# Optimization experiments

Measured on AMD Instinct MI355X. Metric: run time of the kernel, lower is better.

## Reference

```python
import jax, jax.numpy as jnp
import numpy as np

jax.config.update("jax_enable_x64", True)  # original torch code runs in float64; minors underflow fp32

D = 96   # Nsites
N = 48   # Nparticles


def setup_inputs() -> dict:
    key = jax.random.key(0)
    # Orthonormal single-particle orbitals (columns), as the module assumes (P^T P = I)
    A = jax.random.normal(key, (D, D), dtype=jnp.float64)
    Q, _ = jnp.linalg.qr(A)
    P = Q[:, :N]  # [D, N]
    # A valid ordered particle configuration: strictly increasing, occ_positions[k] <= D-N+k
    occ_positions = jnp.arange(N, dtype=jnp.int32) * (D // N)  # stride-2 filling
    return {"P": P, "occ_positions": occ_positions}


def _cond_probs(P, occ_positions):
    """Conditional probabilities probs[k, x] of placing the k-th (ordered) particle at
    site x given particles 0..k-1 at occ_positions[0..k-1].

    Math identical to SlaterDetSampler_ordered.get_cond_prob (naive_update=True):
      G = I - P P^T
      probs[k,x] = -det(M_x[0:x+1,0:x+1]) / det(M[0:xmin,0:xmin])
    where M = G - diag(occupancy of particles < k) and M_x additionally sets n_x = 1.
    Since Ksites is always the contiguous range 0..x, all determinants are LEADING
    principal minors; and because only the (x,x) diagonal entry changes by -1 (last index
    of the block), det(M_x block) = d_{x+1} - d_x with d_j the leading j-minor of M.
    """
    Dd, Nn = P.shape
    dt = P.dtype
    eye = jnp.eye(Dd, dtype=dt)
    G = eye - P @ P.T                                             # [D, D]

    onehots = jax.nn.one_hot(occ_positions, Dd, dtype=dt)         # [N, D]
    n_before = jnp.cumsum(onehots, axis=0) - onehots              # occupancy of particles < k
    A = G[None] - n_before[:, :, None] * eye                      # [N, D, D]: G - diag(n_<k)

    # All leading principal minors via batched det of masked matrices:
    # M_j = A on the [0:j,0:j] block, identity elsewhere  =>  det(M_j) = leading j-minor
    ii = jnp.arange(Dd)
    jj = jnp.arange(1, Dd + 1)
    blk = (ii[None, :, None] < jj[:, None, None]) & (ii[None, None, :] < jj[:, None, None])  # [D,D,D]
    Ms = jnp.where(blk[None], A[:, None], eye)                    # [N, D, D, D]
    d = jnp.linalg.det(Ms.reshape(Nn * Dd, Dd, Dd)).reshape(Nn, Dd)
    d_full = jnp.concatenate([jnp.ones((Nn, 1), dt), d], axis=1)  # d_full[k, j] = j-th leading minor

    k = jnp.arange(Nn)
    xmin = jnp.where(k == 0, 0, occ_positions[jnp.maximum(k - 1, 0)] + 1)  # [N]
    xmax = Dd - Nn + k + 1                                                  # [N]
    denom = jnp.take_along_axis(d_full, xmin[:, None], axis=1)              # [N, 1]
    num = d_full[:, 1:] - d_full[:, :-1]                                    # det(GG_num) per candidate x

    x = jnp.arange(Dd)
    support = (x[None, :] >= xmin[:, None]) & (x[None, :] < xmax[:, None])
    probs = jnp.where(support, -num / denom, jnp.zeros((), dt))
    # torch.where(abs(probs) > 1e-15, probs, 0.)
    probs = jnp.where(jnp.abs(probs) > 1e-15, probs, jnp.zeros((), dt))
    return probs


def reference(P, occ_positions):
    probs = _cond_probs(P, occ_positions)                          # [N, D]
    # prob of the full ordered sample = prod_k probs[k, occ_positions[k]]  (as in sample())
    p_k = jnp.take_along_axis(probs, occ_positions[:, None], axis=1)[:, 0]
    prob_sample = jnp.prod(p_k)
    return probs, prob_sample
```

## Files before the change

kernel.cpp:

```cpp
#include <hip/hip_runtime.h>
#include <math.h>

#define Dd 96
#define Nn 48
#define LD 97
#define PTS 98
#define WS_G_BYTES (Dd * Dd * 8)

__device__ __forceinline__ double frcp(double x) {
    double r = __builtin_amdgcn_rcp(x);
    r = fma(fma(-x, r, 1.0), r, r);
    r = fma(fma(-x, r, 1.0), r, r);
    return r;
}

__device__ __forceinline__ double rdlane(double v, int srcLane) {
    union { double d; int i[2]; } u; u.d = v;
    int lo = __builtin_amdgcn_readlane(u.i[0], srcLane);
    int hi = __builtin_amdgcn_readlane(u.i[1], srcLane);
    union { int i[2]; double d; } w; w.i[0] = lo; w.i[1] = hi;
    return w.d;
}

__global__ __launch_bounds__(256) void build_g(const float* __restrict__ P,
                                               double* __restrict__ Mg) {
    __shared__ float Ps[Dd * 48];
    const int t0 = threadIdx.x;
    for (int e = t0; e < Dd * 48; e += 256) Ps[e] = P[e];
    __syncthreads();
    const int e = blockIdx.x * 256 + t0;
    const int r = e / Dd, c = e - Dd * (e / Dd);
    const float* pr = Ps + r * 48;
    const float* pc = Ps + c * 48;
    double acc = 0.0;
#pragma unroll
    for (int t = 0; t < 48; ++t)
        acc -= (double)pr[t] * (double)pc[t];
    Mg[e] = acc;
}

__global__ __launch_bounds__(1024, 1) void slater_elim(const double* __restrict__ Mg,
                                                       const int* __restrict__ occ,
                                                       float* __restrict__ out,
                                                       unsigned* __restrict__ cnt) {
    __shared__ double Sbuf[4][6][Dd];
    __shared__ double ev16[16][6];
    __shared__ int    evmask16[16], sdead16[16];
    __shared__ double evm[6];
    __shared__ int    evmmask;
    __shared__ double gs_runprod;
    __shared__ int    gs_dead;
    __shared__ int    step_pub;
    __shared__ int    done4[4];
    __shared__ unsigned char flag[Dd];

    const int tid  = threadIdx.x;
    const int k    = blockIdx.x;
    const int n    = Dd - Nn + k + 1;
    const int lane = tid & 63;
    const int wave = tid >> 6;
    const int xmin = (k == 0) ? 0 : occ[k - 1] + 1;
    const int s_end = (n - 1) / 6;
    const int jend  = 6 * s_end;

    if (tid == 0) { step_pub = -1; gs_runprod = 1.0; gs_dead = 0; evmmask = 0; }
    if (tid < 4)  done4[tid] = 0;
    if (tid < 16) { evmask16[tid] = 0; sdead16[tid] = 0; }
    if (tid < Dd) flag[tid] = 0;
    __syncthreads();
    if (tid < k) flag[occ[tid]] = 1;
    __syncthreads();

    double myprob = 0.0;
    double rr[6][2];

#pragma unroll
    for (int u = 0; u < 6; ++u) {
        if (lane < 48) {
            const int row = 6 * wave + u;
            double2 g = *(const double2*)(Mg + row * Dd + 2 * lane);
            double d0 = (row == 2 * lane     && !flag[row]) ? 1.0 : 0.0;
            double d1 = (row == 2 * lane + 1 && !flag[row]) ? 1.0 : 0.0;
            rr[u][0] = g.x + d0;
            rr[u][1] = g.y + d1;
        } else { rr[u][0] = 0.0; rr[u][1] = 0.0; }
    }

    auto prefactor = [&](int p, int slot) {
        const int jb = 6 * p, jbH = 3 * p;
        double grun = gs_runprod; int gdead = gs_dead;
        int msk = 0;
#pragma unroll
        for (int cc = 0; cc < 6; ++cc) {
            const int src = jbH + (cc >> 1);
            double piv = rdlane(rr[cc][cc & 1], src);
            if (!gdead) {
                double ap = fabs(piv);
                int jj = jb + cc;
                if (jj >= xmin) {
                    if (lane == 0) ev16[p][cc] = grun * (1.0 - piv);
                    msk |= (1 << cc);
                    double nr = grun * piv;
                    if (!(ap > 1e-7) || !(ap < 8.0) || !(fabs(nr) > 1e-8)) gdead = 1;
                    else grun = nr;
                } else {
                    if (!(ap > 1e-12) || !(ap < 8.0)) gdead = 1;
                }
            }
            double rp = frcp(piv);
            rr[cc][0] *= rp; rr[cc][1] *= rp;
#pragma unroll
            for (int i = 0; i < 6; ++i) {
                if (i == cc) continue;
                double f = rdlane(rr[i][cc & 1], src);
                rr[i][0] -= f * rr[cc][0];
                rr[i][1] -= f * rr[cc][1];
            }
        }
        if (lane == 0) {
            evmask16[p] = msk; sdead16[p] = gdead;
            gs_runprod = grun; gs_dead = gdead;
        }
        if (lane < 48) {
            const bool live = (2 * lane >= jb + 6);
#pragma unroll
            for (int r = 0; r < 6; ++r) {
                double2 sv;
                sv.x = live ? rr[r][0] : 0.0;
                sv.y = live ? rr[r][1] : 0.0;
                *(double2*)&Sbuf[slot][r][2 * lane] = sv;
            }
        }
        __threadfence_block();
        if (lane == 0)
            __hip_atomic_store(&step_pub, p, __ATOMIC_RELEASE, __HIP_MEMORY_SCOPE_WORKGROUP);
    };

    if (wave == 0) prefactor(0, 0);

    bool broke = false;
    const int smax = (wave < s_end) ? wave : s_end;
    for (int s = 0; s < smax; ++s) {
        while (__hip_atomic_load(&step_pub, __ATOMIC_ACQUIRE,
                                 __HIP_MEMORY_SCOPE_WORKGROUP) < s)
            __builtin_amdgcn_s_sleep(1);
        if (sdead16[s]) { broke = true; break; }
        const int slot = s & 3;
        double S0[6], S1[6];
        if (lane < 48) {
#pragma unroll
            for (int r = 0; r < 6; ++r) {
                double2 sv = *(const double2*)&Sbuf[slot][r][2 * lane];
                S0[r] = sv.x; S1[r] = sv.y;
            }
        }
        asm volatile("s_waitcnt lgkmcnt(0)" ::: "memory");
        if (lane == 0)
            __hip_atomic_fetch_add(&done4[slot], 1, __ATOMIC_RELAXED,
                                   __HIP_MEMORY_SCOPE_WORKGROUP);
        if (lane < 48) {
            const int al = 3 * s;
#pragma unroll
            for (int u = 0; u < 6; ++u) {
#pragma unroll
                for (int r = 0; r < 6; ++r) {
                    double a = rdlane(rr[u][r & 1], al + (r >> 1));
                    rr[u][0] -= a * S0[r];
                    rr[u][1] -= a * S1[r];
                }
            }
        }
        if (wave == s + 1 && s + 1 < s_end) {
            const int p = s + 1;
            if (p >= 4) {
                const int q = p & 3, m = p >> 2;
                const int T = m * (15 - q) - 2 * m * (m - 1);
                while (__hip_atomic_load(&done4[q], __ATOMIC_ACQUIRE,
                                         __HIP_MEMORY_SCOPE_WORKGROUP) < T)
                    __builtin_amdgcn_s_sleep(1);
            }
            prefactor(p, p & 3);
        }
    }

    if (!broke && wave == s_end) {
        const int rsz = n - jend;
        double grun = gs_runprod; int gdead = gs_dead;
        int msk = 0;
#pragma unroll
        for (int cc = 0; cc < 6; ++cc) {
            const int src = 3 * s_end + (cc >> 1);
            double piv = rdlane(rr[cc][cc & 1], src);
            double evv = 0.0;
            if (cc < rsz - 1) {
                if (!gdead) {
                    double ap = fabs(piv);
                    int jj = jend + cc;
                    if (jj >= xmin) {
                        evv = grun * (1.0 - piv); msk |= (1 << cc);
                        double nr = grun * piv;
                        if (!(ap > 1e-7) || !(ap < 8.0) || !(fabs(nr) > 1e-8)) gdead = 1;
                        else grun = nr;
                    } else {
                        if (!(ap > 1e-12) || !(ap < 8.0)) gdead = 1;
                    }
                }
            } else if (cc == rsz - 1) {
                if (!gdead) { evv = grun * (1.0 - piv); msk |= (1 << cc); }
            }
            if (lane == 0) evm[cc] = evv;
            double rp = frcp(piv);
            rr[cc][0] *= rp; rr[cc][1] *= rp;
#pragma unroll
            for (int i = 0; i < 6; ++i) {
                if (i == cc) continue;
                double f = rdlane(rr[i][cc & 1], src);
                rr[i][0] -= f * rr[cc][0];
                rr[i][1] -= f * rr[cc][1];
            }
        }
        if (lane == 0) evmmask = msk;
    }
    __syncthreads();

    if (tid < jend) {
        int sp = tid / 6, q = tid - 6 * sp;
        if ((evmask16[sp] >> q) & 1) myprob = ev16[sp][q];
    } else if (tid < n) {
        int q = tid - jend;
        if ((evmmask >> q) & 1) myprob = evm[q];
    }

    if (tid < Dd) {
        double p = myprob;
        if (!isfinite(p)) p = 0.0;
        if (!(fabs(p) > 1e-15)) p = 0.0;
        p = fmin(fmax(p, 0.0), 1.0);
        out[k * Dd + tid] = (float)p;
    }

    __threadfence();
    __syncthreads();
    if (wave == 0) {
        int old = 0;
        if (lane == 0)
            old = (int)__hip_atomic_fetch_add(cnt, 1u, __ATOMIC_ACQ_REL,
                                              __HIP_MEMORY_SCOPE_AGENT);
        old = __shfl(old, 0, 64);
        if (((unsigned)old + 1u) % (unsigned)Nn == 0u) {
            __threadfence();
            double v = 1.0;
            if (lane < Nn) {
                float f = __hip_atomic_load(out + lane * Dd + occ[lane],
                                            __ATOMIC_RELAXED, __HIP_MEMORY_SCOPE_AGENT);
                v = (double)f;
            }
#pragma unroll
            for (int off = 32; off >= 1; off >>= 1)
                v *= __shfl_down(v, off, 64);
            if (lane == 0) {
                if (!isfinite(v)) v = 0.0;
                out[Nn * Dd] = (float)v;
            }
        }
    }
}

__global__ __launch_bounds__(1024, 1) void slater_mono(const float* __restrict__ P,
                                                       const int* __restrict__ occ,
                                                       float* __restrict__ out,
                                                       unsigned* __restrict__ cnt) {
    __shared__ double As[Dd * LD];
    __shared__ double Sbuf[4][6][Dd];
    __shared__ double ev16[16][6];
    __shared__ int    evmask16[16], sdead16[16];
    __shared__ double evm[6];
    __shared__ int    evmmask;
    __shared__ double gs_runprod;
    __shared__ int    gs_dead;
    __shared__ int    step_pub;
    __shared__ int    done4[4];
    __shared__ unsigned char flag[Dd];
    float* PT = (float*)As;

    const int tid  = threadIdx.x;
    const int k    = blockIdx.x;
    const int n    = Dd - Nn + k + 1;
    const int lane = tid & 63;
    const int wave = tid >> 6;
    const int xmin = (k == 0) ? 0 : occ[k - 1] + 1;
    const int s_end = (n - 1) / 6;
    const int jend  = 6 * s_end;

    if (tid == 0) { step_pub = -1; gs_runprod = 1.0; gs_dead = 0; evmmask = 0; }
    if (tid < 4)  done4[tid] = 0;
    if (tid < 16) { evmask16[tid] = 0; sdead16[tid] = 0; }
    if (tid < Dd) flag[tid] = 0;
    __syncthreads();
    if (tid < k) flag[occ[tid]] = 1;
    for (int e = tid; e < Dd * Nn; e += 1024) {
        int c = e / Nn, t = e - (e / Nn) * Nn;
        PT[t * PTS + c] = P[e];
    }
    __syncthreads();

    double Areg[8]; int trs[2], tcs[2];
#pragma unroll
    for (int it = 0; it < 2; ++it) {
        int tau = tid + 1024 * it;
        double s00 = 0.0, s01 = 0.0, s10 = 0.0, s11 = 0.0;
        int tr = 0, tc = 0;
        if (tau < 1176) {
            tr = (int)((97.0 - sqrt(9409.0 - 8.0 * (double)tau)) * 0.5);
            while ((tr * (97 - tr)) / 2 > tau) --tr;
            while (((tr + 1) * (96 - tr)) / 2 <= tau) ++tr;
            tc = tr + (tau - (tr * (97 - tr)) / 2);
            int r0 = 2 * tr, c0 = 2 * tc;
            if (r0 < n && c0 < n) {
                for (int t = 0; t < Nn; ++t) {
                    const float* row = PT + t * PTS;
                    float2 pr = *(const float2*)(row + r0);
                    float2 pc = *(const float2*)(row + c0);
                    s00 -= (double)pr.x * (double)pc.x; s01 -= (double)pr.x * (double)pc.y;
                    s10 -= (double)pr.y * (double)pc.x; s11 -= (double)pr.y * (double)pc.y;
                }
            }
        }
        trs[it] = tr; tcs[it] = tc;
        Areg[it * 4 + 0] = s00; Areg[it * 4 + 1] = s01;
        Areg[it * 4 + 2] = s10; Areg[it * 4 + 3] = s11;
    }
    __syncthreads();
#pragma unroll
    for (int it = 0; it < 2; ++it) {
        int tau = tid + 1024 * it;
        if (tau < 1176) {
            int tr = trs[it], tc = tcs[it];
            int r0 = 2 * tr, c0 = 2 * tc;
            if (r0 < n && c0 < n) {
                bool r1 = (r0 + 1 < n), c1 = (c0 + 1 < n);
                double d0 = flag[r0] ? 0.0 : 1.0;
                double d1 = flag[r0 + 1] ? 0.0 : 1.0;
                As[r0 * LD + c0] = Areg[it * 4 + 0] + ((r0 == c0) ? d0 : 0.0);
                if (c1)       As[r0 * LD + c0 + 1]       = Areg[it * 4 + 1];
                if (r1)       As[(r0 + 1) * LD + c0]     = Areg[it * 4 + 2];
                if (r1 && c1) As[(r0 + 1) * LD + c0 + 1] = Areg[it * 4 + 3] + ((r0 == c0) ? d1 : 0.0);
                if (tr != tc) {
                    As[c0 * LD + r0] = Areg[it * 4 + 0];
                    if (c1)       As[(c0 + 1) * LD + r0]     = Areg[it * 4 + 1];
                    if (r1)       As[c0 * LD + r0 + 1]       = Areg[it * 4 + 2];
                    if (r1 && c1) As[(c0 + 1) * LD + r0 + 1] = Areg[it * 4 + 3];
                }
            }
        }
    }
    __syncthreads();

    double myprob = 0.0;
    double rr[6][2];
#pragma unroll
    for (int u = 0; u < 6; ++u) {
        if (lane < 48) {
            rr[u][0] = As[(6 * wave + u) * LD + 2 * lane];
            rr[u][1] = As[(6 * wave + u) * LD + 2 * lane + 1];
        } else { rr[u][0] = 0.0; rr[u][1] = 0.0; }
    }

    auto prefactor = [&](int p, int slot) {
        const int jb = 6 * p, jbH = 3 * p;
        double grun = gs_runprod; int gdead = gs_dead;
        int msk = 0;
#pragma unroll
        for (int cc = 0; cc < 6; ++cc) {
            const int src = jbH + (cc >> 1);
            double piv = rdlane(rr[cc][cc & 1], src);
            if (!gdead) {
                double ap = fabs(piv);
                int jj = jb + cc;
                if (jj >= xmin) {
                    if (lane == 0) ev16[p][cc] = grun * (1.0 - piv);
                    msk |= (1 << cc);
                    double nr = grun * piv;
                    if (!(ap > 1e-7) || !(ap < 8.0) || !(fabs(nr) > 1e-8)) gdead = 1;
                    else grun = nr;
                } else {
                    if (!(ap > 1e-12) || !(ap < 8.0)) gdead = 1;
                }
            }
            double rp = frcp(piv);
            rr[cc][0] *= rp; rr[cc][1] *= rp;
#pragma unroll
            for (int i = 0; i < 6; ++i) {
                if (i == cc) continue;
                double f = rdlane(rr[i][cc & 1], src);
                rr[i][0] -= f * rr[cc][0];
                rr[i][1] -= f * rr[cc][1];
            }
        }
        if (lane == 0) {
            evmask16[p] = msk; sdead16[p] = gdead;
            gs_runprod = grun; gs_dead = gdead;
        }
        if (lane < 48) {
            const bool live = (2 * lane >= jb + 6);
#pragma unroll
            for (int r = 0; r < 6; ++r) {
                double2 sv;
                sv.x = live ? rr[r][0] : 0.0;
                sv.y = live ? rr[r][1] : 0.0;
                *(double2*)&Sbuf[slot][r][2 * lane] = sv;
            }
        }
        __threadfence_block();
        if (lane == 0)
            __hip_atomic_store(&step_pub, p, __ATOMIC_RELEASE, __HIP_MEMORY_SCOPE_WORKGROUP);
    };

    if (wave == 0) prefactor(0, 0);

    bool broke = false;
    const int smax = (wave < s_end) ? wave : s_end;
    for (int s = 0; s < smax; ++s) {
        while (__hip_atomic_load(&step_pub, __ATOMIC_ACQUIRE,
                                 __HIP_MEMORY_SCOPE_WORKGROUP) < s)
            __builtin_amdgcn_s_sleep(1);
        if (sdead16[s]) { broke = true; break; }
        const int slot = s & 3;
        double S0[6], S1[6];
        if (lane < 48) {
#pragma unroll
            for (int r = 0; r < 6; ++r) {
                double2 sv = *(const double2*)&Sbuf[slot][r][2 * lane];
                S0[r] = sv.x; S1[r] = sv.y;
            }
        }
        asm volatile("s_waitcnt lgkmcnt(0)" ::: "memory");
        if (lane == 0)
            __hip_atomic_fetch_add(&done4[slot], 1, __ATOMIC_RELAXED,
                                   __HIP_MEMORY_SCOPE_WORKGROUP);
        if (lane < 48) {
            const int al = 3 * s;
#pragma unroll
            for (int u = 0; u < 6; ++u) {
#pragma unroll
                for (int r = 0; r < 6; ++r) {
                    double a = rdlane(rr[u][r & 1], al + (r >> 1));
                    rr[u][0] -= a * S0[r];
                    rr[u][1] -= a * S1[r];
                }
            }
        }
        if (wave == s + 1 && s + 1 < s_end) {
            const int p = s + 1;
            if (p >= 4) {
                const int q = p & 3, m = p >> 2;
                const int T = m * (15 - q) - 2 * m * (m - 1);
                while (__hip_atomic_load(&done4[q], __ATOMIC_ACQUIRE,
                                         __HIP_MEMORY_SCOPE_WORKGROUP) < T)
                    __builtin_amdgcn_s_sleep(1);
            }
            prefactor(p, p & 3);
        }
    }

    if (!broke && wave == s_end) {
        const int rsz = n - jend;
        double grun = gs_runprod; int gdead = gs_dead;
        int msk = 0;
#pragma unroll
        for (int cc = 0; cc < 6; ++cc) {
            const int src = 3 * s_end + (cc >> 1);
            double piv = rdlane(rr[cc][cc & 1], src);
            double evv = 0.0;
            if (cc < rsz - 1) {
                if (!gdead) {
                    double ap = fabs(piv);
                    int jj = jend + cc;
                    if (jj >= xmin) {
                        evv = grun * (1.0 - piv); msk |= (1 << cc);
                        double nr = grun * piv;
                        if (!(ap > 1e-7) || !(ap < 8.0) || !(fabs(nr) > 1e-8)) gdead = 1;
                        else grun = nr;
                    } else {
                        if (!(ap > 1e-12) || !(ap < 8.0)) gdead = 1;
                    }
                }
            } else if (cc == rsz - 1) {
                if (!gdead) { evv = grun * (1.0 - piv); msk |= (1 << cc); }
            }
            if (lane == 0) evm[cc] = evv;
            double rp = frcp(piv);
            rr[cc][0] *= rp; rr[cc][1] *= rp;
#pragma unroll
            for (int i = 0; i < 6; ++i) {
                if (i == cc) continue;
                double f = rdlane(rr[i][cc & 1], src);
                rr[i][0] -= f * rr[cc][0];
                rr[i][1] -= f * rr[cc][1];
            }
        }
        if (lane == 0) evmmask = msk;
    }
    __syncthreads();

    if (tid < jend) {
        int sp = tid / 6, q = tid - 6 * sp;
        if ((evmask16[sp] >> q) & 1) myprob = ev16[sp][q];
    } else if (tid < n) {
        int q = tid - jend;
        if ((evmmask >> q) & 1) myprob = evm[q];
    }

    if (tid < Dd) {
        double p = myprob;
        if (!isfinite(p)) p = 0.0;
        if (!(fabs(p) > 1e-15)) p = 0.0;
        p = fmin(fmax(p, 0.0), 1.0);
        out[k * Dd + tid] = (float)p;
    }

    __threadfence();
    __syncthreads();
    if (wave == 0) {
        int old = 0;
        if (lane == 0)
            old = (int)__hip_atomic_fetch_add(cnt, 1u, __ATOMIC_ACQ_REL,
                                              __HIP_MEMORY_SCOPE_AGENT);
        old = __shfl(old, 0, 64);
        if (((unsigned)old + 1u) % (unsigned)Nn == 0u) {
            __threadfence();
            double v = 1.0;
            if (lane < Nn) {
                float f = __hip_atomic_load(out + lane * Dd + occ[lane],
                                            __ATOMIC_RELAXED, __HIP_MEMORY_SCOPE_AGENT);
                v = (double)f;
            }
#pragma unroll
            for (int off = 32; off >= 1; off >>= 1)
                v *= __shfl_down(v, off, 64);
            if (lane == 0) {
                if (!isfinite(v)) v = 0.0;
                out[Nn * Dd] = (float)v;
            }
        }
    }
}

extern "C" void kernel_launch(void* const* d_in, const int* in_sizes, int n_in,
                              void* d_out, int out_size, void* d_ws, size_t ws_size,
                              hipStream_t stream) {
    const float* P = (const float*)d_in[0];
    const int* occ = (const int*)d_in[1];
    float* out = (float*)d_out;

    if (ws_size >= (size_t)(WS_G_BYTES + 16)) {
        double* Mg = (double*)d_ws;
        unsigned* cnt = (unsigned*)((char*)d_ws + WS_G_BYTES);
        build_g<<<36, 256, 0, stream>>>(P, Mg);
        slater_elim<<<Nn, 1024, 0, stream>>>(Mg, occ, out, cnt);
    } else {
        slater_mono<<<Nn, 1024, 0, stream>>>(P, occ, out, (unsigned*)d_ws);
    }
}
```

Baseline: 93.64 us.

## Widen elimination panels to 12 rows per wave with 512-thread blocks

Restructures the pipelined blocked Gaussian elimination so each wave owns 12 matrix rows instead of 6, using 8 waves per block instead of 16. This halves the number of sequential panel-factorization steps and the cross-wave handoffs through shared memory. The trailing update now runs in four 3-row chunks of the published panel, which keeps register pressure down. In exchange, each serial prefactor step does roughly four times the work, and the done-counter wait threshold is rewritten for the new schedule, which could be wrong.

```diff
diff --git a/kernel.cpp b/kernel.cpp
--- a/kernel.cpp
+++ b/kernel.cpp
@@ -39,14 +39,14 @@
     Mg[e] = acc;
 }
 
-__global__ __launch_bounds__(1024, 1) void slater_elim(const double* __restrict__ Mg,
-                                                       const int* __restrict__ occ,
-                                                       float* __restrict__ out,
-                                                       unsigned* __restrict__ cnt) {
-    __shared__ double Sbuf[4][6][Dd];
-    __shared__ double ev16[16][6];
-    __shared__ int    evmask16[16], sdead16[16];
-    __shared__ double evm[6];
+__global__ __launch_bounds__(512, 1) void slater_elim12(const double* __restrict__ Mg,
+                                                        const int* __restrict__ occ,
+                                                        float* __restrict__ out,
+                                                        unsigned* __restrict__ cnt) {
+    __shared__ double Sbuf[4][12][Dd];
+    __shared__ double ev8[8][12];
+    __shared__ int    evmask8[8], sdead8[8];
+    __shared__ double evm[12];
     __shared__ int    evmmask;
     __shared__ double gs_runprod;
     __shared__ int    gs_dead;
@@ -60,24 +60,24 @@
     const int lane = tid & 63;
     const int wave = tid >> 6;
     const int xmin = (k == 0) ? 0 : occ[k - 1] + 1;
-    const int s_end = (n - 1) / 6;
-    const int jend  = 6 * s_end;
+    const int s_end = (n - 1) / 12;
+    const int jend  = 12 * s_end;
 
     if (tid == 0) { step_pub = -1; gs_runprod = 1.0; gs_dead = 0; evmmask = 0; }
     if (tid < 4)  done4[tid] = 0;
-    if (tid < 16) { evmask16[tid] = 0; sdead16[tid] = 0; }
+    if (tid < 8)  { evmask8[tid] = 0; sdead8[tid] = 0; }
     if (tid < Dd) flag[tid] = 0;
     __syncthreads();
     if (tid < k) flag[occ[tid]] = 1;
     __syncthreads();
 
     double myprob = 0.0;
-    double rr[6][2];
-
-#pragma unroll
-    for (int u = 0; u < 6; ++u) {
-        if (lane < 48) {
-            const int row = 6 * wave + u;
+    double rr[12][2];
+
+#pragma unroll
+    for (int u = 0; u < 12; ++u) {
+        if (lane < 48) {
+            const int row = 12 * wave + u;
             double2 g = *(const double2*)(Mg + row * Dd + 2 * lane);
             double d0 = (row == 2 * lane     && !flag[row]) ? 1.0 : 0.0;
             double d1 = (row == 2 * lane + 1 && !flag[row]) ? 1.0 : 0.0;
@@ -87,18 +87,18 @@
     }
 
     auto prefactor = [&](int p, int slot) {
-        const int jb = 6 * p, jbH = 3 * p;
+        const int jb = 12 * p, jbH = 6 * p;
         double grun = gs_runprod; int gdead = gs_dead;
         int msk = 0;
 #pragma unroll
-        for (int cc = 0; cc < 6; ++cc) {
+        for (int cc = 0; cc < 12; ++cc) {
             const int src = jbH + (cc >> 1);
             double piv = rdlane(rr[cc][cc & 1], src);
             if (!gdead) {
                 double ap = fabs(piv);
                 int jj = jb + cc;
                 if (jj >= xmin) {
-                    if (lane == 0) ev16[p][cc] = grun * (1.0 - piv);
+                    if (lane == 0) ev8[p][cc] = grun * (1.0 - piv);
                     msk |= (1 << cc);
                     double nr = grun * piv;
                     if (!(ap > 1e-7) || !(ap < 8.0) || !(fabs(nr) > 1e-8)) gdead = 1;
@@ -110,7 +110,7 @@
             double rp = frcp(piv);
             rr[cc][0] *= rp; rr[cc][1] *= rp;
 #pragma unroll
-            for (int i = 0; i < 6; ++i) {
+            for (int i = 0; i < 12; ++i) {
                 if (i == cc) continue;
                 double f = rdlane(rr[i][cc & 1], src);
                 rr[i][0] -= f * rr[cc][0];
@@ -118,13 +118,13 @@
             }
         }
         if (lane == 0) {
-            evmask16[p] = msk; sdead16[p] = gdead;
+            evmask8[p] = msk; sdead8[p] = gdead;
             gs_runprod = grun; gs_dead = gdead;
         }
         if (lane < 48) {
-            const bool live = (2 * lane >= jb + 6);
-#pragma unroll
-            for (int r = 0; r < 6; ++r) {
+            const bool live = (lane >= 6 * (p + 1));
+#pragma unroll
+            for (int r = 0; r < 12; ++r) {
                 double2 sv;
                 sv.x = live ? rr[r][0] : 0.0;
                 sv.y = live ? rr[r][1] : 0.0;
@@ -144,39 +144,39 @@
         while (__hip_atomic_load(&step_pub, __ATOMIC_ACQUIRE,
                                  __HIP_MEMORY_SCOPE_WORKGROUP) < s)
             __builtin_amdgcn_s_sleep(1);
-        if (sdead16[s]) { broke = true; break; }
+        if (sdead8[s]) { broke = true; break; }
         const int slot = s & 3;
-        double S0[6], S1[6];
-        if (lane < 48) {
-#pragma unroll
-            for (int r = 0; r < 6; ++r) {
-                double2 sv = *(const double2*)&Sbuf[slot][r][2 * lane];
-                S0[r] = sv.x; S1[r] = sv.y;
+        if (lane < 48) {
+            const int al = 6 * s;
+#pragma unroll
+            for (int qd = 0; qd < 4; ++qd) {
+                double S0[3], S1[3];
+#pragma unroll
+                for (int r = 0; r < 3; ++r) {
+                    double2 sv = *(const double2*)&Sbuf[slot][3 * qd + r][2 * lane];
+                    S0[r] = sv.x; S1[r] = sv.y;
+                }
+#pragma unroll
+                for (int u = 0; u < 12; ++u) {
+#pragma unroll
+                    for (int r = 0; r < 3; ++r) {
+                        const int rg = 3 * qd + r;
+                        double a = rdlane(rr[u][rg & 1], al + (rg >> 1));
+                        rr[u][0] -= a * S0[r];
+                        rr[u][1] -= a * S1[r];
+                    }
+                }
             }
         }
         asm volatile("s_waitcnt lgkmcnt(0)" ::: "memory");
         if (lane == 0)
             __hip_atomic_fetch_add(&done4[slot], 1, __ATOMIC_RELAXED,
                                    __HIP_MEMORY_SCOPE_WORKGROUP);
-        if (lane < 48) {
-            const int al = 3 * s;
-#pragma unroll
-            for (int u = 0; u < 6; ++u) {
-#pragma unroll
-                for (int r = 0; r < 6; ++r) {
-                    double a = rdlane(rr[u][r & 1], al + (r >> 1));
-                    rr[u][0] -= a * S0[r];
-                    rr[u][1] -= a * S1[r];
-                }
-            }
-        }
         if (wave == s + 1 && s + 1 < s_end) {
             const int p = s + 1;
             if (p >= 4) {
-                const int q = p & 3, m = p >> 2;
-                const int T = m * (15 - q) - 2 * m * (m - 1);
-                while (__hip_atomic_load(&done4[q], __ATOMIC_ACQUIRE,
-                                         __HIP_MEMORY_SCOPE_WORKGROUP) < T)
+                while (__hip_atomic_load(&done4[p & 3], __ATOMIC_ACQUIRE,
+                                         __HIP_MEMORY_SCOPE_WORKGROUP) < 11 - p)
                     __builtin_amdgcn_s_sleep(1);
             }
             prefactor(p, p & 3);
@@ -188,8 +188,8 @@
         double grun = gs_runprod; int gdead = gs_dead;
         int msk = 0;
 #pragma unroll
-        for (int cc = 0; cc < 6; ++cc) {
-            const int src = 3 * s_end + (cc >> 1);
+        for (int cc = 0; cc < 12; ++cc) {
+            const int src = 6 * s_end + (cc >> 1);
             double piv = rdlane(rr[cc][cc & 1], src);
             double evv = 0.0;
             if (cc < rsz - 1) {
@@ -212,7 +212,7 @@
             double rp = frcp(piv);
             rr[cc][0] *= rp; rr[cc][1] *= rp;
 #pragma unroll
-            for (int i = 0; i < 6; ++i) {
+            for (int i = 0; i < 12; ++i) {
                 if (i == cc) continue;
                 double f = rdlane(rr[i][cc & 1], src);
                 rr[i][0] -= f * rr[cc][0];
@@ -224,8 +224,8 @@
     __syncthreads();
 
     if (tid < jend) {
-        int sp = tid / 6, q = tid - 6 * sp;
-        if ((evmask16[sp] >> q) & 1) myprob = ev16[sp][q];
+        int sp = tid / 12, q = tid - 12 * sp;
+        if ((evmask8[sp] >> q) & 1) myprob = ev8[sp][q];
     } else if (tid < n) {
         int q = tid - jend;
         if ((evmmask >> q) & 1) myprob = evm[q];
@@ -557,7 +557,7 @@
         double* Mg = (double*)d_ws;
         unsigned* cnt = (unsigned*)((char*)d_ws + WS_G_BYTES);
         build_g<<<36, 256, 0, stream>>>(P, Mg);
-        slater_elim<<<Nn, 1024, 0, stream>>>(Mg, occ, out, cnt);
+        slater_elim12<<<Nn, 512, 0, stream>>>(Mg, occ, out, cnt);
     } else {
         slater_mono<<<Nn, 1024, 0, stream>>>(P, occ, out, (unsigned*)d_ws);
     }
```

Result: slower. 102.2 us (+9.2%).
